# Performance work log

Hardware: AMD Instinct MI355X
Metric: run time of the kernel (lower is better)

Reference implementation:

```python
import math
import jax, jax.numpy as jnp
import numpy as np

B, T, S, H, L, NH = 2, 512, 2048, 768, 32, 12
INTERMED = 4 * H


def _make_pe(max_len, hidden):
    position = np.arange(max_len)[:, None].astype(np.float32)
    div_term = np.exp(np.arange(0, hidden, 2).astype(np.float32) * (-math.log(10000.0) / hidden))
    pe = np.zeros((max_len, hidden), dtype=np.float32)
    pe[:, 0::2] = np.sin(position * div_term)
    pe[:, 1::2] = np.cos(position * div_term)
    return jnp.asarray(pe)


def setup_inputs() -> dict:
    key = jax.random.key(0)
    ks = jax.random.split(key, 10)
    token_reps = jax.random.normal(ks[0], (B, T, H), dtype=jnp.float32)
    starts = jax.random.randint(ks[1], (B, S), 0, T - L)
    lens = jax.random.randint(ks[2], (B, S), 1, L + 1)
    span_ids = jnp.stack([starts, starts + lens], axis=-1)  # (B,S,2)
    span_masks = jax.random.uniform(ks[3], (B, S)) > 0.2
    pe = _make_pe(T, H)
    dummy_query = jax.random.normal(ks[4], (H,), dtype=jnp.float32) * 0.02
    in_proj_w = jax.random.normal(ks[5], (3 * H, H), dtype=jnp.float32) * 0.02
    in_proj_b = jnp.zeros((3 * H,), jnp.float32)
    out_proj_w = jax.random.normal(ks[6], (H, H), dtype=jnp.float32) * 0.02
    out_proj_b = jnp.zeros((H,), jnp.float32)
    norm_g = jnp.ones((H,), jnp.float32)
    norm_b = jnp.zeros((H,), jnp.float32)
    ffn_w1 = jax.random.normal(ks[7], (INTERMED, H), dtype=jnp.float32) * (math.sqrt(2.0 / H))
    ffn_b1 = jnp.zeros((INTERMED,), jnp.float32)
    ffn_w2 = jax.random.normal(ks[8], (H, INTERMED), dtype=jnp.float32) * (math.sqrt(2.0 / INTERMED))
    ffn_b2 = jnp.zeros((H,), jnp.float32)
    return dict(token_reps=token_reps, span_ids=span_ids, span_masks=span_masks,
                pooling=0, pe=pe, dummy_query=dummy_query,
                in_proj_w=in_proj_w, in_proj_b=in_proj_b,
                out_proj_w=out_proj_w, out_proj_b=out_proj_b,
                norm_g=norm_g, norm_b=norm_b,
                ffn_w1=ffn_w1, ffn_b1=ffn_b1, ffn_w2=ffn_w2, ffn_b2=ffn_b2)


def _layernorm(x, g, b, eps=1e-5):
    mu = jnp.mean(x, axis=-1, keepdims=True)
    var = jnp.mean(jnp.square(x - mu), axis=-1, keepdims=True)
    return (x - mu) * jax.lax.rsqrt(var + eps) * g + b


def reference(token_reps, span_ids, span_masks, pooling, pe, dummy_query,
              in_proj_w, in_proj_b, out_proj_w, out_proj_b,
              norm_g, norm_b, ffn_w1, ffn_b1, ffn_w2, ffn_b2):
    b, t, h = token_reps.shape
    s = span_ids.shape[1]
    hd = h // NH
    # positional encoding over the sequence (dropout=0 / eval mode)
    x = token_reps + pe[:t]
    # ragged -> padded gather of span tokens
    starts = span_ids[..., 0]
    lens = (span_ids[..., 1] - starts) * span_masks.astype(span_ids.dtype)  # (B,S)
    ar = jnp.arange(L)
    pos = starts[..., None] + ar                     # (B,S,L)
    valid = ar[None, None, :] < lens[..., None]      # (B,S,L) True = real token
    idx = jnp.clip(pos, 0, t - 1)
    gathered = jax.vmap(lambda xb, ib: xb[ib])(x, idx)   # (B,S,L,H)
    gathered = gathered * valid[..., None]
    # guard fully-masked rows (masked-out / zero-len spans): keep one key valid,
    # output is zeroed at the end anyway (matches torch span_reps[~mask]=0)
    any_v = jnp.any(valid, axis=-1)
    valid = valid.at[..., 0].set(valid[..., 0] | ~any_v)
    # single-query multi-head attention (torch nn.MultiheadAttention math)
    Wq, Wk, Wv = jnp.split(in_proj_w, 3, axis=0)
    bq, bk, bv = jnp.split(in_proj_b, 3, axis=0)
    q = (dummy_query @ Wq.T + bq).reshape(NH, hd)                  # (NH,hd)
    k = (gathered @ Wk.T + bk).reshape(b, s, L, NH, hd)
    v = (gathered @ Wv.T + bv).reshape(b, s, L, NH, hd)
    scores = jnp.einsum('nd,bslnd->bsnl', q, k) / math.sqrt(hd)    # (B,S,NH,L)
    scores = jnp.where(valid[:, :, None, :], scores, -jnp.inf)
    attn = jax.nn.softmax(scores, axis=-1)
    ctx = jnp.einsum('bsnl,bslnd->bsnd', attn, v).reshape(b, s, h)
    attn_out = ctx @ out_proj_w.T + out_proj_b
    # residual + LayerNorm, FFN, residual + same LayerNorm
    x1 = _layernorm(attn_out + dummy_query, norm_g, norm_b)
    ffn = jax.nn.relu(x1 @ ffn_w1.T + ffn_b1) @ ffn_w2.T + ffn_b2
    out = _layernorm(ffn + x1, norm_g, norm_b)
    out = out * span_masks[..., None]
    return out
```

## Files before the change

### kernel.cpp

```cpp
#include <hip/hip_runtime.h>
#include <math.h>

static constexpr int B_  = 2;
static constexpr int T_  = 512;
static constexpr int S_  = 2048;
static constexpr int H_  = 768;
static constexpr int L_  = 32;
static constexpr int NH_ = 12;
static constexpr int HD_ = 64;
static constexpr int IM_ = 3072;

typedef __bf16 bf16x8 __attribute__((ext_vector_type(8)));
typedef float  f32x4  __attribute__((ext_vector_type(4)));

__device__ __forceinline__ float bf2f(unsigned short u) {
    return __uint_as_float(((unsigned)u) << 16);
}
__device__ __forceinline__ unsigned short f2bf(float f) {
    unsigned u = __float_as_uint(f);
    u += 0x7fffu + ((u >> 16) & 1u);
    return (unsigned short)(u >> 16);
}
__device__ __forceinline__ void gl_lds16(const void* g, void* l) {
    __builtin_amdgcn_global_load_lds((const __attribute__((address_space(1))) void*)g,
                                     (__attribute__((address_space(3))) void*)l, 16, 0, 0);
}

__global__ void k_mask(const int* __restrict__ raw, int* __restrict__ mout) {
    __shared__ int bad;
    if (threadIdx.x == 0) bad = 0;
    __syncthreads();
    int v = raw[threadIdx.x];
    if (v != 0 && v != 1) bad = 1;
    __syncthreads();
    int byte_layout = bad;
    const unsigned char* rb = (const unsigned char*)raw;
    for (int i = threadIdx.x; i < B_ * S_; i += 1024)
        mout[i] = byte_layout ? (int)rb[i] : raw[i];
}

__global__ void k_q(const float* __restrict__ dq, const float* __restrict__ w,
                    const float* __restrict__ b, float* __restrict__ q) {
    int wv = threadIdx.x >> 6, lane = threadIdx.x & 63;
    int i = blockIdx.x * 4 + wv;
    const float* row = w + (size_t)i * H_;
    float acc = 0.f;
#pragma unroll
    for (int k = 0; k < 12; ++k) acc += dq[lane + 64 * k] * row[lane + 64 * k];
    for (int m = 32; m; m >>= 1) acc += __shfl_xor(acc, m, 64);
    if (lane == 0) q[i] = acc + b[i];
}

__global__ void k_wqeff(const float* __restrict__ q, const float* __restrict__ w,
                        float* __restrict__ wq) {
    int i = blockIdx.x * 256 + threadIdx.x;
    if (i >= NH_ * H_) return;
    int n = i / H_, hh = i % H_;
    float acc = 0.f;
    for (int d = 0; d < HD_; ++d)
        acc += q[n * HD_ + d] * w[(size_t)(H_ + n * HD_ + d) * H_ + hh];
    wq[i] = acc;
}

__global__ void k_castw(const float* __restrict__ s0, const float* __restrict__ s1,
                        const float* __restrict__ s2, const float* __restrict__ s3,
                        unsigned short* __restrict__ d0, unsigned short* __restrict__ d1,
                        unsigned short* __restrict__ d2, unsigned short* __restrict__ d3) {
    const long n0 = (long)H_ * H_, n2 = (long)IM_ * H_;
    long gid = (long)(blockIdx.x * 256 + threadIdx.x) * 8;
    const float* s; unsigned short* d; long off;
    if (gid < n0)                { s = s0; d = d0; off = gid; }
    else if (gid < 2 * n0)       { s = s1; d = d1; off = gid - n0; }
    else if (gid < 2 * n0 + n2)  { s = s2; d = d2; off = gid - 2 * n0; }
    else                         { s = s3; d = d3; off = gid - 2 * n0 - n2; }
    float4 f0 = *(const float4*)(s + off);
    float4 f1 = *(const float4*)(s + off + 4);
    uint4 o;
    o.x = (unsigned)f2bf(f0.x) | ((unsigned)f2bf(f0.y) << 16);
    o.y = (unsigned)f2bf(f0.z) | ((unsigned)f2bf(f0.w) << 16);
    o.z = (unsigned)f2bf(f1.x) | ((unsigned)f2bf(f1.y) << 16);
    o.w = (unsigned)f2bf(f1.z) | ((unsigned)f2bf(f1.w) << 16);
    *(uint4*)(d + off) = o;
}

__global__ void k_castv2(const float* __restrict__ p0, const float* __restrict__ p1,
                         unsigned short* __restrict__ dst, int n) {
    int i = (blockIdx.x * 256 + threadIdx.x) * 8;
    if (i >= n) return;
    float4 a0 = *(const float4*)(p0 + i);
    float4 a1 = *(const float4*)(p0 + i + 4);
    float4 b0 = *(const float4*)(p1 + i);
    float4 b1 = *(const float4*)(p1 + i + 4);
    uint4 o;
    o.x = (unsigned)f2bf(a0.x + b0.x) | ((unsigned)f2bf(a0.y + b0.y) << 16);
    o.y = (unsigned)f2bf(a0.z + b0.z) | ((unsigned)f2bf(a0.w + b0.w) << 16);
    o.z = (unsigned)f2bf(a1.x + b1.x) | ((unsigned)f2bf(a1.y + b1.y) << 16);
    o.w = (unsigned)f2bf(a1.z + b1.z) | ((unsigned)f2bf(a1.w + b1.w) << 16);
    *(uint4*)(dst + i) = o;
}

__global__ void k_addpe(const float* __restrict__ tr, const float* __restrict__ pe,
                        unsigned short* __restrict__ x) {
    int i = (blockIdx.x * 256 + threadIdx.x) * 8;
    if (i >= B_ * T_ * H_) return;
    float4 a0 = *(const float4*)(tr + i);
    float4 a1 = *(const float4*)(tr + i + 4);
    const float* pp = pe + (i % (T_ * H_));
    float4 p0 = *(const float4*)pp;
    float4 p1 = *(const float4*)(pp + 4);
    uint4 o;
    o.x = (unsigned)f2bf(a0.x + p0.x) | ((unsigned)f2bf(a0.y + p0.y) << 16);
    o.y = (unsigned)f2bf(a0.z + p0.z) | ((unsigned)f2bf(a0.w + p0.w) << 16);
    o.z = (unsigned)f2bf(a1.x + p1.x) | ((unsigned)f2bf(a1.y + p1.y) << 16);
    o.w = (unsigned)f2bf(a1.z + p1.z) | ((unsigned)f2bf(a1.w + p1.w) << 16);
    *(uint4*)(x + i) = o;
}

__global__ void k_stok(const unsigned short* __restrict__ x, const float* __restrict__ wq,
                       float* __restrict__ stok) {
    int bt = blockIdx.x;
    int lane = threadIdx.x & 63, w = threadIdx.x >> 6;
    const unsigned short* xr = x + (size_t)bt * H_;
    float xv[12];
#pragma unroll
    for (int k = 0; k < 12; ++k) xv[k] = bf2f(xr[lane + 64 * k]);
#pragma unroll
    for (int hh = 0; hh < 3; ++hh) {
        int n = w * 3 + hh;
        const float* wr = wq + (size_t)n * H_;
        float acc = 0.f;
#pragma unroll
        for (int k = 0; k < 12; ++k) acc += xv[k] * wr[lane + 64 * k];
        for (int m = 32; m; m >>= 1) acc += __shfl_xor(acc, m, 64);
        if (lane == 0) stok[bt * NH_ + n] = acc;
    }
}

template <bool RELU, bool OBF, bool SPLIT>
__global__ __launch_bounds__(256)
void gemm_bt(const unsigned short* __restrict__ A, const unsigned short* __restrict__ W,
             const float* __restrict__ bias, void* __restrict__ Cout,
             int M, int N, int K, int kLen) {
    __shared__ unsigned short As[8192];
    __shared__ unsigned short Bs[8192];
    const int bm = blockIdx.y * 128, bn = blockIdx.x * 128;
    const int kOff = blockIdx.z * kLen;
    const int tid = threadIdx.x, lane = tid & 63, wid = tid >> 6;
    const int wm = (wid >> 1) * 64, wn = (wid & 1) * 64;
    const int r8 = lane >> 3, c8 = lane & 7;
    const int swc = (c8 ^ r8) * 8;
    const unsigned short* agp = A + (size_t)(bm + wid * 32 + r8) * K + kOff + swc;
    const unsigned short* bgp = W + (size_t)(bn + wid * 32 + r8) * K + kOff + swc;
    unsigned short* lA = As + wid * 2048;
    unsigned short* lB = Bs + wid * 2048;

    f32x4 acc[4][4];
#pragma unroll
    for (int i = 0; i < 4; ++i)
#pragma unroll
        for (int j = 0; j < 4; ++j) acc[i][j] = f32x4{0.f, 0.f, 0.f, 0.f};

    const int mrow = lane & 15;
    const int l7 = lane & 7;
    const int cq0 = lane >> 4;
    const int NIT = kLen >> 6;

    for (int it = 0; it < NIT; ++it) {
        const int k0 = it << 6;
#pragma unroll
        for (int j = 0; j < 4; ++j) {
            gl_lds16(agp + (size_t)(8 * j) * K + k0, lA + j * 512);
            gl_lds16(bgp + (size_t)(8 * j) * K + k0, lB + j * 512);
        }
        __syncthreads();
        bf16x8 af[2][4], bfr[2][4];
#pragma unroll
        for (int s = 0; s < 2; ++s) {
            const int cq = s * 4 + cq0;
            const int sw = (cq ^ l7) * 8;
#pragma unroll
            for (int i = 0; i < 4; ++i)
                af[s][i] = *(const bf16x8*)(As + (wm + i * 16 + mrow) * 64 + sw);
#pragma unroll
            for (int j = 0; j < 4; ++j)
                bfr[s][j] = *(const bf16x8*)(Bs + (wn + j * 16 + mrow) * 64 + sw);
        }
#pragma unroll
        for (int s = 0; s < 2; ++s)
#pragma unroll
            for (int i = 0; i < 4; ++i)
#pragma unroll
                for (int j = 0; j < 4; ++j)
                    acc[i][j] = __builtin_amdgcn_mfma_f32_16x16x32_bf16(af[s][i], bfr[s][j], acc[i][j], 0, 0, 0);
        __syncthreads();
    }

    const bool addb = !SPLIT || blockIdx.z == 0;
    float* outp = SPLIT ? ((float*)Cout) + (size_t)blockIdx.z * M * N : (float*)Cout;
    const int lr = (lane >> 4) * 4, lc = lane & 15;
#pragma unroll
    for (int j = 0; j < 4; ++j) {
        int col = bn + wn + j * 16 + lc;
        float bv = addb ? bias[col] : 0.f;
#pragma unroll
        for (int i = 0; i < 4; ++i) {
            int row0 = bm + wm + i * 16 + lr;
#pragma unroll
            for (int r = 0; r < 4; ++r) {
                float v = acc[i][j][r] + bv;
                if (RELU) v = fmaxf(v, 0.f);
                if (OBF)
                    ((unsigned short*)Cout)[(size_t)(row0 + r) * N + col] = f2bf(v);
                else
                    outp[(size_t)(row0 + r) * N + col] = v;
            }
        }
    }
}

__global__ void k_attn(const float* __restrict__ stok, const unsigned short* __restrict__ vtok,
                       const int* __restrict__ span_ids, const int* __restrict__ masks,
                       unsigned short* __restrict__ ctx) {
    int r = blockIdx.x, b = r / S_;
    unsigned short* out = ctx + (size_t)r * H_;
    int tid = threadIdx.x;
    __shared__ float w[NH_][L_];
    __shared__ int idxs[L_];
    __shared__ int s_len;
    if (tid == 0) {
        int m = masks[r];
        int st = span_ids[2 * r], en = span_ids[2 * r + 1];
        int len = m ? (en - st) : 0;
        len = len < 0 ? 0 : (len > L_ ? L_ : len);
        s_len = len;
    }
    __syncthreads();
    int len = s_len;
    if (len == 0) {
        for (int h2 = tid; h2 < H_ / 2; h2 += 256) ((unsigned*)out)[h2] = 0u;
        return;
    }
    if (tid < L_) {
        int p = span_ids[2 * r] + tid;
        idxs[tid] = p < 0 ? 0 : (p > T_ - 1 ? T_ - 1 : p);
    }
    __syncthreads();
    for (int i = tid; i < NH_ * L_; i += 256) {
        int n = i / L_, l = i % L_;
        w[n][l] = (l < len) ? stok[(size_t)(b * T_ + idxs[l]) * NH_ + n] * 0.125f : -INFINITY;
    }
    __syncthreads();
    if (tid < NH_) {
        float mx = -INFINITY;
        for (int l = 0; l < len; ++l) mx = fmaxf(mx, w[tid][l]);
        float sum = 0.f;
        for (int l = 0; l < len; ++l) { float e = __expf(w[tid][l] - mx); w[tid][l] = e; sum += e; }
        float inv = 1.f / sum;
        for (int l = 0; l < len; ++l) w[tid][l] *= inv;
    }
    __syncthreads();
    if (tid < 192) {
        int h0 = tid * 4, n = h0 >> 6;
        float a0 = 0.f, a1 = 0.f, a2 = 0.f, a3 = 0.f;
        for (int l = 0; l < len; ++l) {
            float wl = w[n][l];
            const unsigned short* vr = vtok + (size_t)(b * T_ + idxs[l]) * H_ + h0;
            uint2 u = *(const uint2*)vr;
            a0 += wl * bf2f((unsigned short)(u.x & 0xffff));
            a1 += wl * bf2f((unsigned short)(u.x >> 16));
            a2 += wl * bf2f((unsigned short)(u.y & 0xffff));
            a3 += wl * bf2f((unsigned short)(u.y >> 16));
        }
        uint2 o;
        o.x = (unsigned)f2bf(a0) | ((unsigned)f2bf(a1) << 16);
        o.y = (unsigned)f2bf(a2) | ((unsigned)f2bf(a3) << 16);
        *(uint2*)(out + h0) = o;
    }
}

template <bool RESROW, bool MASKOUT>
__global__ void k_ln(const float* __restrict__ parts, size_t pstr,
                     const float* __restrict__ resf, const unsigned short* __restrict__ resb,
                     const float* __restrict__ g, const float* __restrict__ bt,
                     float* __restrict__ outf, unsigned short* __restrict__ outb,
                     const int* __restrict__ masks) {
    int r = blockIdx.x;
    const float* p0 = parts + (size_t)r * H_;
    const float* p1 = parts + pstr + (size_t)r * H_;
    int tid = threadIdx.x;
    float v[3];
    float lsum = 0.f;
#pragma unroll
    for (int i = 0; i < 3; ++i) {
        int h = tid + 256 * i;
        float res = RESROW ? bf2f(resb[(size_t)r * H_ + h]) : resf[h];
        v[i] = p0[h] + p1[h] + res;
        lsum += v[i];
    }
    __shared__ float sh[256];
    sh[tid] = lsum;
    __syncthreads();
    for (int st = 128; st > 0; st >>= 1) {
        if (tid < st) sh[tid] += sh[tid + st];
        __syncthreads();
    }
    float mean = sh[0] * (1.f / H_);
    __syncthreads();
    float lvar = 0.f;
#pragma unroll
    for (int i = 0; i < 3; ++i) { float d = v[i] - mean; lvar += d * d; }
    sh[tid] = lvar;
    __syncthreads();
    for (int st = 128; st > 0; st >>= 1) {
        if (tid < st) sh[tid] += sh[tid + st];
        __syncthreads();
    }
    float var = sh[0] * (1.f / H_);
    float scale = rsqrtf(var + 1e-5f);
    float mfac = 1.f;
    if (MASKOUT) mfac = masks[r] ? 1.f : 0.f;
#pragma unroll
    for (int i = 0; i < 3; ++i) {
        int h = tid + 256 * i;
        float o = ((v[i] - mean) * scale * g[h] + bt[h]) * mfac;
        if (MASKOUT) outf[(size_t)r * H_ + h] = o;
        else         outb[(size_t)r * H_ + h] = f2bf(o);
    }
}

extern "C" void kernel_launch(void* const* d_in, const int* in_sizes, int n_in,
                              void* d_out, int out_size, void* d_ws, size_t ws_size,
                              hipStream_t stream) {
    const float* token_reps = (const float*)d_in[0];
    const int*   span_ids   = (const int*)d_in[1];
    const int*   masks_raw  = (const int*)d_in[2];
    const float* pe   = (const float*)d_in[4];
    const float* dq   = (const float*)d_in[5];
    const float* in_w = (const float*)d_in[6];
    const float* in_b = (const float*)d_in[7];
    const float* ow   = (const float*)d_in[8];
    const float* ob   = (const float*)d_in[9];
    const float* g    = (const float*)d_in[10];
    const float* bt   = (const float*)d_in[11];
    const float* w1   = (const float*)d_in[12];
    const float* b1   = (const float*)d_in[13];
    const float* w2   = (const float*)d_in[14];
    const float* b2   = (const float*)d_in[15];

    const int BS = B_ * S_;
    const int BT = B_ * T_;

    float* fws   = (float*)d_ws;
    float* stok  = fws;
    float* qv    = stok + BT * NH_;
    float* wqeff = qv + H_;
    float* big   = wqeff + NH_ * H_;
    unsigned short* us   = (unsigned short*)(big + (size_t)2 * BS * H_);
    unsigned short* xbf  = us;
    unsigned short* vtok = xbf + (size_t)BT * H_;
    unsigned short* ctx  = vtok + (size_t)BT * H_;
    unsigned short* x1bf = ctx + (size_t)BS * H_;
    unsigned short* f1   = x1bf + (size_t)BS * H_;
    unsigned short* wvb  = f1 + (size_t)BS * IM_;
    unsigned short* owb  = wvb + H_ * H_;
    unsigned short* w1b  = owb + H_ * H_;
    unsigned short* w2b  = w1b + IM_ * H_;
    int* maskn = (int*)(w2b + H_ * IM_);

    k_mask<<<1, 1024, 0, stream>>>(masks_raw, maskn);
    k_q<<<H_ / 4, 256, 0, stream>>>(dq, in_w, in_b, qv);
    k_wqeff<<<(NH_ * H_ + 255) / 256, 256, 0, stream>>>(qv, in_w, wqeff);
    {
        long total8 = ((long)2 * H_ * H_ + (long)2 * IM_ * H_) / 8;
        k_castw<<<(int)(total8 / 256), 256, 0, stream>>>(
            in_w + (size_t)2 * H_ * H_, ow, w1, w2, wvb, owb, w1b, w2b);
    }
    k_addpe<<<(BT * H_ / 8 + 255) / 256, 256, 0, stream>>>(token_reps, pe, xbf);
    k_stok<<<BT, 256, 0, stream>>>(xbf, wqeff, stok);
    {
        dim3 grid(H_ / 128, BT / 128, 2);
        gemm_bt<false, false, true><<<grid, 256, 0, stream>>>(
            xbf, wvb, in_b + 2 * H_, big, BT, H_, H_, H_ / 2);
        k_castv2<<<(BT * H_ / 8 + 255) / 256, 256, 0, stream>>>(
            big, big + (size_t)BT * H_, vtok, BT * H_);
    }
    k_attn<<<BS, 256, 0, stream>>>(stok, vtok, span_ids, maskn, ctx);
    {
        dim3 grid(H_ / 128, BS / 128, 2);
        gemm_bt<false, false, true><<<grid, 256, 0, stream>>>(
            ctx, owb, ob, big, BS, H_, H_, H_ / 2);
    }
    k_ln<false, false><<<BS, 256, 0, stream>>>(
        big, (size_t)BS * H_, dq, nullptr, g, bt, nullptr, x1bf, nullptr);
    {
        dim3 grid(IM_ / 128, BS / 128, 1);
        gemm_bt<true, true, false><<<grid, 256, 0, stream>>>(
            x1bf, w1b, b1, f1, BS, IM_, H_, H_);
    }
    {
        dim3 grid(H_ / 128, BS / 128, 2);
        gemm_bt<false, false, true><<<grid, 256, 0, stream>>>(
            f1, w2b, b2, big, BS, H_, IM_, IM_ / 2);
    }
    k_ln<true, true><<<BS, 256, 0, stream>>>(
        big, (size_t)BS * H_, nullptr, x1bf, g, bt, (float*)d_out, nullptr, maskn);
}
```

Before: 254.2 us.

## Use 4-way split-K with bf16 partials and remap GEMM blocks into 8-wide column groups

```diff
diff --git a/kernel.cpp b/kernel.cpp
--- a/kernel.cpp
+++ b/kernel.cpp
@@ -83,20 +83,23 @@
     *(uint4*)(d + off) = o;
 }
 
-__global__ void k_castv2(const float* __restrict__ p0, const float* __restrict__ p1,
+__global__ void k_castv4(const unsigned short* __restrict__ p, size_t pstr,
                          unsigned short* __restrict__ dst, int n) {
-    int i = (blockIdx.x * 256 + threadIdx.x) * 8;
+    int i = (blockIdx.x * 256 + threadIdx.x) * 4;
     if (i >= n) return;
-    float4 a0 = *(const float4*)(p0 + i);
-    float4 a1 = *(const float4*)(p0 + i + 4);
-    float4 b0 = *(const float4*)(p1 + i);
-    float4 b1 = *(const float4*)(p1 + i + 4);
-    uint4 o;
-    o.x = (unsigned)f2bf(a0.x + b0.x) | ((unsigned)f2bf(a0.y + b0.y) << 16);
-    o.y = (unsigned)f2bf(a0.z + b0.z) | ((unsigned)f2bf(a0.w + b0.w) << 16);
-    o.z = (unsigned)f2bf(a1.x + b1.x) | ((unsigned)f2bf(a1.y + b1.y) << 16);
-    o.w = (unsigned)f2bf(a1.z + b1.z) | ((unsigned)f2bf(a1.w + b1.w) << 16);
-    *(uint4*)(dst + i) = o;
+    float a0 = 0.f, a1 = 0.f, a2 = 0.f, a3 = 0.f;
+#pragma unroll
+    for (int z = 0; z < 4; ++z) {
+        uint2 u = *(const uint2*)(p + z * pstr + i);
+        a0 += bf2f((unsigned short)(u.x & 0xffff));
+        a1 += bf2f((unsigned short)(u.x >> 16));
+        a2 += bf2f((unsigned short)(u.y & 0xffff));
+        a3 += bf2f((unsigned short)(u.y >> 16));
+    }
+    uint2 o;
+    o.x = (unsigned)f2bf(a0) | ((unsigned)f2bf(a1) << 16);
+    o.y = (unsigned)f2bf(a2) | ((unsigned)f2bf(a3) << 16);
+    *(uint2*)(dst + i) = o;
 }
 
 __global__ void k_addpe(const float* __restrict__ tr, const float* __restrict__ pe,
@@ -136,15 +139,21 @@
     }
 }
 
-template <bool RELU, bool OBF, bool SPLIT>
+template <bool RELU, bool SPLIT>
 __global__ __launch_bounds__(256)
 void gemm_bt(const unsigned short* __restrict__ A, const unsigned short* __restrict__ W,
-             const float* __restrict__ bias, void* __restrict__ Cout,
-             int M, int N, int K, int kLen) {
+             const float* __restrict__ bias, unsigned short* __restrict__ Cout,
+             int M, int N, int K, int kLen, int TX, int SP) {
     __shared__ unsigned short As[8192];
     __shared__ unsigned short Bs[8192];
-    const int bm = blockIdx.y * 128, bn = blockIdx.x * 128;
-    const int kOff = blockIdx.z * kLen;
+    const int qx = blockIdx.x & 7, t = blockIdx.x >> 3;
+    const int gi = t / TX, x = t - gi * TX;
+    const int g = gi * 8 + qx;
+    int y, z;
+    if (SPLIT) { y = g / SP; z = g - y * SP; } else { y = g; z = 0; }
+    const int bm = y * 128, bn = x * 128;
+    const int kOff = z * kLen;
+
     const int tid = threadIdx.x, lane = tid & 63, wid = tid >> 6;
     const int wm = (wid >> 1) * 64, wn = (wid & 1) * 64;
     const int r8 = lane >> 3, c8 = lane & 7;
@@ -195,8 +204,8 @@
         __syncthreads();
     }
 
-    const bool addb = !SPLIT || blockIdx.z == 0;
-    float* outp = SPLIT ? ((float*)Cout) + (size_t)blockIdx.z * M * N : (float*)Cout;
+    const bool addb = !SPLIT || z == 0;
+    unsigned short* outp = SPLIT ? Cout + (size_t)z * M * N : Cout;
     const int lr = (lane >> 4) * 4, lc = lane & 15;
 #pragma unroll
     for (int j = 0; j < 4; ++j) {
@@ -209,10 +218,7 @@
             for (int r = 0; r < 4; ++r) {
                 float v = acc[i][j][r] + bv;
                 if (RELU) v = fmaxf(v, 0.f);
-                if (OBF)
-                    ((unsigned short*)Cout)[(size_t)(row0 + r) * N + col] = f2bf(v);
-                else
-                    outp[(size_t)(row0 + r) * N + col] = v;
+                outp[(size_t)(row0 + r) * N + col] = f2bf(v);
             }
         }
     }
@@ -279,23 +285,24 @@
 }
 
 template <bool RESROW, bool MASKOUT>
-__global__ void k_ln(const float* __restrict__ parts, size_t pstr,
+__global__ void k_ln(const unsigned short* __restrict__ parts, size_t pstr,
                      const float* __restrict__ resf, const unsigned short* __restrict__ resb,
                      const float* __restrict__ g, const float* __restrict__ bt,
                      float* __restrict__ outf, unsigned short* __restrict__ outb,
                      const int* __restrict__ masks) {
     int r = blockIdx.x;
-    const float* p0 = parts + (size_t)r * H_;
-    const float* p1 = parts + pstr + (size_t)r * H_;
     int tid = threadIdx.x;
     float v[3];
     float lsum = 0.f;
 #pragma unroll
     for (int i = 0; i < 3; ++i) {
         int h = tid + 256 * i;
-        float res = RESROW ? bf2f(resb[(size_t)r * H_ + h]) : resf[h];
-        v[i] = p0[h] + p1[h] + res;
-        lsum += v[i];
+        float s = RESROW ? bf2f(resb[(size_t)r * H_ + h]) : resf[h];
+#pragma unroll
+        for (int z = 0; z < 4; ++z)
+            s += bf2f(parts[z * pstr + (size_t)r * H_ + h]);
+        v[i] = s;
+        lsum += s;
     }
     __shared__ float sh[256];
     sh[tid] = lsum;
@@ -354,9 +361,9 @@
     float* stok  = fws;
     float* qv    = stok + BT * NH_;
     float* wqeff = qv + H_;
-    float* big   = wqeff + NH_ * H_;
-    unsigned short* us   = (unsigned short*)(big + (size_t)2 * BS * H_);
-    unsigned short* xbf  = us;
+    unsigned short* us = (unsigned short*)(wqeff + NH_ * H_);
+    unsigned short* pbuf = us;
+    unsigned short* xbf  = pbuf + (size_t)4 * BS * H_;
     unsigned short* vtok = xbf + (size_t)BT * H_;
     unsigned short* ctx  = vtok + (size_t)BT * H_;
     unsigned short* x1bf = ctx + (size_t)BS * H_;
@@ -378,30 +385,20 @@
     k_addpe<<<(BT * H_ / 8 + 255) / 256, 256, 0, stream>>>(token_reps, pe, xbf);
     k_stok<<<BT, 256, 0, stream>>>(xbf, wqeff, stok);
     {
-        dim3 grid(H_ / 128, BT / 128, 2);
-        gemm_bt<false, false, true><<<grid, 256, 0, stream>>>(
-            xbf, wvb, in_b + 2 * H_, big, BT, H_, H_, H_ / 2);
-        k_castv2<<<(BT * H_ / 8 + 255) / 256, 256, 0, stream>>>(
-            big, big + (size_t)BT * H_, vtok, BT * H_);
+        gemm_bt<false, true><<<192, 256, 0, stream>>>(
+            xbf, wvb, in_b + 2 * H_, pbuf, BT, H_, H_, H_ / 4, 6, 4);
+        k_castv4<<<(BT * H_ / 4 + 255) / 256, 256, 0, stream>>>(
+            pbuf, (size_t)BT * H_, vtok, BT * H_);
     }
     k_attn<<<BS, 256, 0, stream>>>(stok, vtok, span_ids, maskn, ctx);
-    {
-        dim3 grid(H_ / 128, BS / 128, 2);
-        gemm_bt<false, false, true><<<grid, 256, 0, stream>>>(
-            ctx, owb, ob, big, BS, H_, H_, H_ / 2);
-    }
+    gemm_bt<false, true><<<768, 256, 0, stream>>>(
+        ctx, owb, ob, pbuf, BS, H_, H_, H_ / 4, 6, 4);
     k_ln<false, false><<<BS, 256, 0, stream>>>(
-        big, (size_t)BS * H_, dq, nullptr, g, bt, nullptr, x1bf, nullptr);
-    {
-        dim3 grid(IM_ / 128, BS / 128, 1);
-        gemm_bt<true, true, false><<<grid, 256, 0, stream>>>(
-            x1bf, w1b, b1, f1, BS, IM_, H_, H_);
-    }
-    {
-        dim3 grid(H_ / 128, BS / 128, 2);
-        gemm_bt<false, false, true><<<grid, 256, 0, stream>>>(
-            f1, w2b, b2, big, BS, H_, IM_, IM_ / 2);
-    }
+        pbuf, (size_t)BS * H_, dq, nullptr, g, bt, nullptr, x1bf, nullptr);
+    gemm_bt<true, false><<<768, 256, 0, stream>>>(
+        x1bf, w1b, b1, f1, BS, IM_, H_, H_, 24, 1);
+    gemm_bt<false, true><<<768, 256, 0, stream>>>(
+        f1, w2b, b2, pbuf, BS, H_, IM_, IM_ / 4, 6, 4);
     k_ln<true, true><<<BS, 256, 0, stream>>>(
-        big, (size_t)BS * H_, nullptr, x1bf, g, bt, (float*)d_out, nullptr, maskn);
-}
+        pbuf, (size_t)BS * H_, nullptr, x1bf, g, bt, (float*)d_out, nullptr, maskn);
+}
```

New measurement: 244.6 us. 3.8% less time.
